# Kernel optimization log

Hardware: AMD Instinct MI355X
Metric: run time of the kernel (lower is better)

## Reference

```python
import jax, jax.numpy as jnp
import numpy as np

DIM = 1024
NUM_HEADS = 16
HEAD_DIM = DIM // NUM_HEADS
BATCH = 2
SEQ = 2048


def setup_inputs() -> dict:
    key = jax.random.key(0)
    ks = jax.random.split(key, 9)
    s = 1.0 / np.sqrt(DIM)  # torch Linear default init scale
    x = jax.random.normal(ks[0], (BATCH, SEQ, DIM), dtype=jnp.float32)
    Wq = jax.random.uniform(ks[1], (DIM, DIM), jnp.float32, -s, s)
    bq = jax.random.uniform(ks[2], (DIM,), jnp.float32, -s, s)
    Wk = jax.random.uniform(ks[3], (DIM, DIM), jnp.float32, -s, s)
    bk = jax.random.uniform(ks[4], (DIM,), jnp.float32, -s, s)
    Wv = jax.random.uniform(ks[5], (DIM, DIM), jnp.float32, -s, s)
    bv = jax.random.uniform(ks[6], (DIM,), jnp.float32, -s, s)
    Wo = jax.random.uniform(ks[7], (DIM, DIM), jnp.float32, -s, s)
    bo = jax.random.uniform(ks[8], (DIM,), jnp.float32, -s, s)
    return {"x": x, "Wq": Wq, "bq": bq, "Wk": Wk, "bk": bk,
            "Wv": Wv, "bv": bv, "Wo": Wo, "bo": bo, "enable_causal": 1}


def reference(x, Wq, bq, Wk, bk, Wv, bv, Wo, bo, enable_causal):
    B, S, D = x.shape
    H, Hd = NUM_HEADS, HEAD_DIM
    # projections (torch Linear: x @ W.T + b; W here stored as [out,in])
    q = (x @ Wq.T + bq).reshape(B, S, H, Hd).transpose(0, 2, 1, 3)  # [B,H,S,Hd]
    k = (x @ Wk.T + bk).reshape(B, S, H, Hd).transpose(0, 2, 1, 3)
    v = (x @ Wv.T + bv).reshape(B, S, H, Hd).transpose(0, 2, 1, 3)
    scores = jnp.einsum('bhqd,bhkd->bhqk', q, k) / np.sqrt(Hd)  # [B,H,S,S]
    if enable_causal:
        causal = jnp.triu(jnp.ones((S, S), dtype=bool), k=1)
        scores = jnp.where(causal, -jnp.inf, scores)
    attn = jax.nn.softmax(scores, axis=-1)
    # dropout p=0.0 -> identity (eval-mode math)
    out = jnp.einsum('bhqk,bhkd->bhqd', attn, v)  # [B,H,S,Hd]
    out = out.transpose(0, 2, 1, 3).reshape(B, S, D)
    return out @ Wo.T + bo
```

## Files before the change

### kernel.cpp

```cpp
#include <hip/hip_runtime.h>
#include <hip/hip_bf16.h>
#include <stdint.h>

typedef unsigned short u16;
typedef short bf16x8 __attribute__((ext_vector_type(8)));
typedef float f32x4 __attribute__((ext_vector_type(4)));

#define S_LEN   2048
#define D_MODEL 1024
#define NH      16
#define M_TOK   4096
#define LOG2E   1.4426950408889634f

__device__ __forceinline__ u16 f2b(float f) {
  union { float f; unsigned int u; } v; v.f = f;
  unsigned int r = v.u + 0x7FFFu + ((v.u >> 16) & 1u);
  return (u16)(r >> 16);
}

__device__ __forceinline__ float exp2_fast(float x) {
  float r;
  asm("v_exp_f32 %0, %1" : "=v"(r) : "v"(x));
  return r;
}

__device__ __forceinline__ void load_lds16(const void* g, void* l) {
  __builtin_amdgcn_global_load_lds(
      (const __attribute__((address_space(1))) void*)g,
      (__attribute__((address_space(3))) void*)l, 16, 0, 0);
}

__global__ __launch_bounds__(256) void k_convert(
    const float* __restrict__ x,
    const float* __restrict__ wq, const float* __restrict__ wk,
    const float* __restrict__ wv, const float* __restrict__ wo,
    u16* __restrict__ xb, u16* __restrict__ wb)
{
  int t = blockIdx.x * 256 + threadIdx.x;
  long e = (long)t * 8;
  const float* src; u16* dst;
  if (e < (long)M_TOK * D_MODEL) { src = x + e; dst = xb + e; }
  else {
    long we = e - (long)M_TOK * D_MODEL;
    int r = (int)(we >> 20);
    long o = we & 1048575;
    const float* ws = (r == 0) ? wq : (r == 1) ? wk : (r == 2) ? wv : wo;
    src = ws + o; dst = wb + ((long)r << 20) + o;
  }
  float4 f0 = *(const float4*)src;
  float4 f1 = *(const float4*)(src + 4);
  u16 u[8];
  u[0] = f2b(f0.x); u[1] = f2b(f0.y); u[2] = f2b(f0.z); u[3] = f2b(f0.w);
  u[4] = f2b(f1.x); u[5] = f2b(f1.y); u[6] = f2b(f1.z); u[7] = f2b(f1.w);
  *(uint4*)dst = *(const uint4*)u;
}

__device__ __forceinline__ void gemm_mainloop(
    const u16* __restrict__ At, const u16* __restrict__ Bt,
    u16* As, u16* Bs, f32x4 acc[4][4])
{
  const int tid  = threadIdx.x;
  const int lane = tid & 63;
  const int w    = tid >> 6;
  const int wr = w >> 1, wc = w & 1;
  const f32x4 fz = {0.f, 0.f, 0.f, 0.f};
  #pragma unroll
  for (int i = 0; i < 4; ++i)
    #pragma unroll
    for (int j = 0; j < 4; ++j) acc[i][j] = fz;

  const int srow = lane >> 3;
  const int sc   = lane & 7;

  for (int k0 = 0; k0 < D_MODEL; k0 += 64) {
    #pragma unroll
    for (int i = 0; i < 4; ++i) {
      int seg = i * 4 + w;
      int row = seg * 8 + srow;
      load_lds16(At + (long)row * D_MODEL + k0 + sc * 8, (char*)As + seg * 1024);
      load_lds16(Bt + (long)row * D_MODEL + k0 + sc * 8, (char*)Bs + seg * 1024);
    }
    __syncthreads();
    #pragma unroll
    for (int kc = 0; kc < 2; ++kc) {
      bf16x8 af[4], bfv[4];
      #pragma unroll
      for (int mi = 0; mi < 4; ++mi) {
        int row = wr * 64 + mi * 16 + (lane & 15);
        af[mi] = *(const bf16x8*)(As + row * 64 + kc * 32 + (lane >> 4) * 8);
      }
      #pragma unroll
      for (int ni = 0; ni < 4; ++ni) {
        int row = wc * 64 + ni * 16 + (lane & 15);
        bfv[ni] = *(const bf16x8*)(Bs + row * 64 + kc * 32 + (lane >> 4) * 8);
      }
      #pragma unroll
      for (int mi = 0; mi < 4; ++mi)
        #pragma unroll
        for (int ni = 0; ni < 4; ++ni)
          acc[mi][ni] = __builtin_amdgcn_mfma_f32_16x16x32_bf16(
              af[mi], bfv[ni], acc[mi][ni], 0, 0, 0);
    }
    __syncthreads();
  }
}

__global__ __launch_bounds__(256) void k_gemm_qkv(
    const u16* __restrict__ xb, const u16* __restrict__ wb,
    const float* __restrict__ bq, const float* __restrict__ bk,
    const float* __restrict__ bv,
    u16* __restrict__ q, u16* __restrict__ k, u16* __restrict__ v)
{
  __shared__ u16 As[128 * 64];
  __shared__ u16 Bs[128 * 64];
  const int m0   = blockIdx.x * 128;
  const int by   = blockIdx.y;
  const int proj = by >> 3;
  const int n0   = (by & 7) * 128;
  f32x4 acc[4][4];
  gemm_mainloop(xb + (long)m0 * D_MODEL,
                wb + (long)proj * 1048576 + (long)n0 * D_MODEL, As, Bs, acc);

  const int lane = threadIdx.x & 63;
  const int w    = threadIdx.x >> 6;
  const int wr = w >> 1, wc = w & 1;
  const float* bias = (proj == 0) ? bq : (proj == 1) ? bk : bv;
  u16* dst = (proj == 0) ? q : (proj == 1) ? k : v;
  const float sc = (proj == 0) ? 0.125f * LOG2E : 1.0f;
  #pragma unroll
  for (int mi = 0; mi < 4; ++mi)
    #pragma unroll
    for (int ni = 0; ni < 4; ++ni) {
      int n = n0 + wc * 64 + ni * 16 + (lane & 15);
      float bval = bias[n];
      int h = n >> 6, d = n & 63;
      #pragma unroll
      for (int r = 0; r < 4; ++r) {
        int m = m0 + wr * 64 + mi * 16 + (lane >> 4) * 4 + r;
        int b = m >> 11, s = m & 2047;
        float val = (acc[mi][ni][r] + bval) * sc;
        dst[(((long)(b * NH + h) * S_LEN + s) << 6) + d] = f2b(val);
      }
    }
}

__global__ __launch_bounds__(256) void k_transpose_v(
    const u16* __restrict__ v, u16* __restrict__ vt)
{
  __shared__ u16 t[64][65];
  const int bh = blockIdx.y;
  const int s0 = blockIdx.x * 64;
  const int tid = threadIdx.x;
  const int r = tid >> 2, cg = tid & 3;
  const u16* src = v + ((long)bh * S_LEN + s0 + r) * 64 + cg * 16;
  uint4 a = *(const uint4*)src;
  uint4 b = *(const uint4*)(src + 8);
  u16 tmp[16];
  *(uint4*)tmp = a; *(uint4*)(tmp + 8) = b;
  #pragma unroll
  for (int j = 0; j < 16; ++j) t[r][cg * 16 + j] = tmp[j];
  __syncthreads();
  u16 o[16];
  #pragma unroll
  for (int j = 0; j < 16; ++j) o[j] = t[cg * 16 + j][r];
  u16* dst = vt + ((long)bh * 64 + r) * S_LEN + s0 + cg * 16;
  *(uint4*)dst = *(const uint4*)o;
  *(uint4*)(dst + 8) = *(const uint4*)(o + 8);
}

__global__ __launch_bounds__(256) void k_attn(
    const u16* __restrict__ Q, const u16* __restrict__ K,
    const u16* __restrict__ Vt, u16* __restrict__ O,
    const int* __restrict__ causal_flag)
{
  __shared__ u16 Ks[2][64 * 64];
  __shared__ u16 Ps[4][16 * 72];

  const int tid  = threadIdx.x;
  const int lane = tid & 63;
  const int w    = tid >> 6;
  const int bid  = blockIdx.x;
  const int xcd  = bid & 7;
  const int j    = bid >> 3;
  const int kk   = j >> 5;
  const int c    = j & 31;
  const int bh   = xcd * 4 + kk;
  const int cc   = (kk & 2) ? ((c + 16) & 31) : c;
  const int qb   = (kk & 1) ? (31 - cc) : cc;
  const int q0   = qb * 64;
  const int causal = *causal_flag;

  const int l15 = lane & 15;
  const int l4  = lane >> 4;

  const u16* Kbh  = K  + (long)bh * S_LEN * 64;
  const u16* Vtbh = Vt + (long)bh * 64 * S_LEN;
  const f32x4 fz = {0.f, 0.f, 0.f, 0.f};
  const int nt = causal ? (qb + 1) : (S_LEN / 64);

  bf16x8 onesv;
  #pragma unroll
  for (int i = 0; i < 8; ++i) onesv[i] = (short)0x3F80;

  const u16 *kg0, *kg1; int lo0, lo1;
  {
    int b0 = w * 64;
    int r0 = (b0 >> 3) + (lane >> 3);
    int c0 = (lane & 7) ^ (r0 & 7);
    kg0 = Kbh + r0 * 64 + c0 * 8;  lo0 = b0 * 16;
    int b1 = 256 + w * 64;
    int r1 = (b1 >> 3) + (lane >> 3);
    int c1 = (lane & 7) ^ (r1 & 7);
    kg1 = Kbh + r1 * 64 + c1 * 8;  lo1 = b1 * 16;
  }
  #define STAGE_T(bufp, toff) do {                                   \
    load_lds16(kg0 + (toff) * 4096, (char*)(bufp) + lo0);            \
    load_lds16(kg1 + (toff) * 4096, (char*)(bufp) + lo1);            \
  } while (0)

  const u16* Vp0 = Vtbh + (long)( 0 + l15) * S_LEN + l4 * 8;
  const u16* Vp1 = Vtbh + (long)(16 + l15) * S_LEN + l4 * 8;
  const u16* Vp2 = Vtbh + (long)(32 + l15) * S_LEN + l4 * 8;
  const u16* Vp3 = Vtbh + (long)(48 + l15) * S_LEN + l4 * 8;

  const u16* Qb = Q + ((long)bh * S_LEN + q0 + w * 16) * 64;
  bf16x8 qf0 = *(const bf16x8*)(Qb + l15 * 64 +      l4 * 8);
  bf16x8 qf1 = *(const bf16x8*)(Qb + l15 * 64 + 32 + l4 * 8);

  f32x4 acc_o[4] = {fz, fz, fz, fz};
  f32x4 acc_l = fz;

  int cur = 0;
  STAGE_T(Ks[0], 0);
  asm volatile("s_waitcnt vmcnt(0)" ::: "memory");
  __builtin_amdgcn_s_barrier();

  #pragma unroll 1
  for (int t = 0; t < nt; ++t) {
    bf16x8 vf0[4], vf1[4];
    vf0[0] = *(const bf16x8*)(Vp0); vf1[0] = *(const bf16x8*)(Vp0 + 32);
    vf0[1] = *(const bf16x8*)(Vp1); vf1[1] = *(const bf16x8*)(Vp1 + 32);
    vf0[2] = *(const bf16x8*)(Vp2); vf1[2] = *(const bf16x8*)(Vp2 + 32);
    vf0[3] = *(const bf16x8*)(Vp3); vf1[3] = *(const bf16x8*)(Vp3 + 32);

    if (t + 1 < nt) STAGE_T(Ks[cur ^ 1], t + 1);

    f32x4 acc_s[4] = {fz, fz, fz, fz};
    __builtin_amdgcn_s_setprio(1);
    #pragma unroll
    for (int kc = 0; kc < 2; ++kc) {
      bf16x8 qf = kc ? qf1 : qf0;
      #pragma unroll
      for (int sub = 0; sub < 4; ++sub) {
        int krow = sub * 16 + l15;
        int cs = (kc * 4 + l4) ^ (krow & 7);
        bf16x8 kf = *(const bf16x8*)(Ks[cur] + krow * 64 + cs * 8);
        acc_s[sub] = __builtin_amdgcn_mfma_f32_16x16x32_bf16(qf, kf, acc_s[sub], 0, 0, 0);
      }
    }
    __builtin_amdgcn_s_setprio(0);

    if (causal && t == nt - 1) {
      #pragma unroll
      for (int sub = 0; sub < 4; ++sub) {
        int kvcol = t * 64 + sub * 16 + l15;
        #pragma unroll
        for (int r = 0; r < 4; ++r) {
          int qrow = q0 + w * 16 + l4 * 4 + r;
          if (kvcol > qrow) acc_s[sub][r] = -1e30f;
        }
      }
    }

    u16* P = &Ps[w][0];
    #pragma unroll
    for (int sub = 0; sub < 4; ++sub)
      #pragma unroll
      for (int r = 0; r < 4; ++r) {
        float p = exp2_fast(acc_s[sub][r]);
        P[(l4 * 4 + r) * 72 + sub * 16 + l15] = f2b(p);
      }

    asm volatile("s_waitcnt lgkmcnt(0)" ::: "memory");
    bf16x8 pf0 = *(const bf16x8*)(P + l15 * 72 +      l4 * 8);
    bf16x8 pf1 = *(const bf16x8*)(P + l15 * 72 + 32 + l4 * 8);
    __builtin_amdgcn_s_setprio(1);
    #pragma unroll
    for (int sub = 0; sub < 4; ++sub) {
      acc_o[sub] = __builtin_amdgcn_mfma_f32_16x16x32_bf16(pf0, vf0[sub], acc_o[sub], 0, 0, 0);
      acc_o[sub] = __builtin_amdgcn_mfma_f32_16x16x32_bf16(pf1, vf1[sub], acc_o[sub], 0, 0, 0);
    }
    acc_l = __builtin_amdgcn_mfma_f32_16x16x32_bf16(pf0, onesv, acc_l, 0, 0, 0);
    acc_l = __builtin_amdgcn_mfma_f32_16x16x32_bf16(pf1, onesv, acc_l, 0, 0, 0);
    __builtin_amdgcn_s_setprio(0);

    if (t + 1 < nt) {
      asm volatile("s_waitcnt vmcnt(0)" ::: "memory");
      __builtin_amdgcn_s_barrier();
      cur ^= 1;
    }
    Vp0 += 64; Vp1 += 64; Vp2 += 64; Vp3 += 64;
  }
  #undef STAGE_T

  const int b = bh >> 4, h = bh & 15;
  float rl[4];
  #pragma unroll
  for (int r = 0; r < 4; ++r) {
    asm("v_rcp_f32 %0, %1" : "=v"(rl[r]) : "v"(acc_l[r]));
  }
  #pragma unroll
  for (int sub = 0; sub < 4; ++sub)
    #pragma unroll
    for (int r = 0; r < 4; ++r) {
      int s = q0 + w * 16 + l4 * 4 + r;
      float val = acc_o[sub][r] * rl[r];
      O[((long)(b * S_LEN + s)) * D_MODEL + h * 64 + sub * 16 + l15] = f2b(val);
    }
}

__global__ __launch_bounds__(256) void k_gemm_o(
    const u16* __restrict__ ob, const u16* __restrict__ wb,
    const float* __restrict__ bo, float* __restrict__ out)
{
  __shared__ u16 As[128 * 64];
  __shared__ u16 Bs[128 * 64];
  const int m0 = blockIdx.x * 128;
  const int n0 = blockIdx.y * 128;
  f32x4 acc[4][4];
  gemm_mainloop(ob + (long)m0 * D_MODEL,
                wb + 3L * 1048576 + (long)n0 * D_MODEL, As, Bs, acc);
  const int lane = threadIdx.x & 63;
  const int w    = threadIdx.x >> 6;
  const int wr = w >> 1, wc = w & 1;
  #pragma unroll
  for (int mi = 0; mi < 4; ++mi)
    #pragma unroll
    for (int ni = 0; ni < 4; ++ni) {
      int n = n0 + wc * 64 + ni * 16 + (lane & 15);
      float bval = bo[n];
      #pragma unroll
      for (int r = 0; r < 4; ++r) {
        int m = m0 + wr * 64 + mi * 16 + (lane >> 4) * 4 + r;
        out[(long)m * D_MODEL + n] = acc[mi][ni][r] + bval;
      }
    }
}

extern "C" void kernel_launch(void* const* d_in, const int* in_sizes, int n_in,
                              void* d_out, int out_size, void* d_ws, size_t ws_size,
                              hipStream_t stream) {
  const float* x  = (const float*)d_in[0];
  const float* Wq = (const float*)d_in[1];
  const float* bq = (const float*)d_in[2];
  const float* Wk = (const float*)d_in[3];
  const float* bk = (const float*)d_in[4];
  const float* Wv = (const float*)d_in[5];
  const float* bv = (const float*)d_in[6];
  const float* Wo = (const float*)d_in[7];
  const float* bo = (const float*)d_in[8];
  const int* causal = (const int*)d_in[9];
  float* out = (float*)d_out;

  char* ws = (char*)d_ws;
  u16* xb = (u16*)(ws);
  u16* wb = (u16*)(ws + (8L  << 20));
  u16* qb = (u16*)(ws + (16L << 20));
  u16* kb = (u16*)(ws + (24L << 20));
  u16* vb = (u16*)(ws + (32L << 20));
  u16* vt = (u16*)(ws + (40L << 20));
  u16* ob = (u16*)(ws);

  k_convert   <<<4096,          256, 0, stream>>>(x, Wq, Wk, Wv, Wo, xb, wb);
  k_gemm_qkv  <<<dim3(32, 24),  256, 0, stream>>>(xb, wb, bq, bk, bv, qb, kb, vb);
  k_transpose_v<<<dim3(32, 32), 256, 0, stream>>>(vb, vt);
  k_attn      <<<1024,          256, 0, stream>>>(qb, kb, vt, ob, causal);
  k_gemm_o    <<<dim3(32, 8),   256, 0, stream>>>(ob, wb, bo, out);
}
```

Before: 251.3 us.

## Fuse V transpose into QKV epilogue and keep attention P in registers

The QKV GEMM epilogue now writes V directly in transposed layout, so the separate transpose kernel and its extra read and write pass are gone. The attention kernel drops the LDS double-buffered K staging and its barriers, loading K fragments straight from global memory into registers. It also computes S transposed (K as the A operand) and rearranges the packed bf16 probabilities across lanes with ds_bpermute instead of an LDS round trip. The cost is more global loads per wave with no sharing of K across waves, and extra cross-lane permute instructions.

```diff
diff --git a/kernel.cpp b/kernel.cpp
--- a/kernel.cpp
+++ b/kernel.cpp
@@ -5,6 +5,7 @@
 typedef unsigned short u16;
 typedef short bf16x8 __attribute__((ext_vector_type(8)));
 typedef float f32x4 __attribute__((ext_vector_type(4)));
+typedef union { unsigned w[4]; bf16x8 v; } pfrag;
 
 #define S_LEN   2048
 #define D_MODEL 1024
@@ -21,6 +22,12 @@
 __device__ __forceinline__ float exp2_fast(float x) {
   float r;
   asm("v_exp_f32 %0, %1" : "=v"(r) : "v"(x));
+  return r;
+}
+
+__device__ __forceinline__ unsigned cvt_pk(float lo, float hi) {
+  unsigned r;
+  asm("v_cvt_pk_bf16_f32 %0, %1, %2" : "=v"(r) : "v"(lo), "v"(hi));
   return r;
 }
 
@@ -109,7 +116,7 @@
     const u16* __restrict__ xb, const u16* __restrict__ wb,
     const float* __restrict__ bq, const float* __restrict__ bk,
     const float* __restrict__ bv,
-    u16* __restrict__ q, u16* __restrict__ k, u16* __restrict__ v)
+    u16* __restrict__ q, u16* __restrict__ k, u16* __restrict__ vt)
 {
   __shared__ u16 As[128 * 64];
   __shared__ u16 Bs[128 * 64];
@@ -125,47 +132,41 @@
   const int w    = threadIdx.x >> 6;
   const int wr = w >> 1, wc = w & 1;
   const float* bias = (proj == 0) ? bq : (proj == 1) ? bk : bv;
-  u16* dst = (proj == 0) ? q : (proj == 1) ? k : v;
   const float sc = (proj == 0) ? 0.125f * LOG2E : 1.0f;
-  #pragma unroll
-  for (int mi = 0; mi < 4; ++mi)
-    #pragma unroll
-    for (int ni = 0; ni < 4; ++ni) {
-      int n = n0 + wc * 64 + ni * 16 + (lane & 15);
-      float bval = bias[n];
-      int h = n >> 6, d = n & 63;
-      #pragma unroll
-      for (int r = 0; r < 4; ++r) {
-        int m = m0 + wr * 64 + mi * 16 + (lane >> 4) * 4 + r;
+
+  if (proj == 2) {
+    #pragma unroll
+    for (int mi = 0; mi < 4; ++mi)
+      #pragma unroll
+      for (int ni = 0; ni < 4; ++ni) {
+        int n = n0 + wc * 64 + ni * 16 + (lane & 15);
+        float bval = bias[n];
+        int h = n >> 6, d = n & 63;
+        int m = m0 + wr * 64 + mi * 16 + (lane >> 4) * 4;
         int b = m >> 11, s = m & 2047;
-        float val = (acc[mi][ni][r] + bval) * sc;
-        dst[(((long)(b * NH + h) * S_LEN + s) << 6) + d] = f2b(val);
-      }
-    }
-}
-
-__global__ __launch_bounds__(256) void k_transpose_v(
-    const u16* __restrict__ v, u16* __restrict__ vt)
-{
-  __shared__ u16 t[64][65];
-  const int bh = blockIdx.y;
-  const int s0 = blockIdx.x * 64;
-  const int tid = threadIdx.x;
-  const int r = tid >> 2, cg = tid & 3;
-  const u16* src = v + ((long)bh * S_LEN + s0 + r) * 64 + cg * 16;
-  uint4 a = *(const uint4*)src;
-  uint4 b = *(const uint4*)(src + 8);
-  u16 tmp[16];
-  *(uint4*)tmp = a; *(uint4*)(tmp + 8) = b;
-  #pragma unroll
-  for (int j = 0; j < 16; ++j) t[r][cg * 16 + j] = tmp[j];
-  __syncthreads();
-  u16 o[16];
-  #pragma unroll
-  for (int j = 0; j < 16; ++j) o[j] = t[cg * 16 + j][r];
-  u16* dst = vt + ((long)bh * 64 + r) * S_LEN + s0 + cg * 16;
-  *(uint4*)dst = *(const uint4*)o;
-  *(uint4*)(dst + 8) = *(const uint4*)(o + 8);
+        u16 o4[4];
+        #pragma unroll
+        for (int r = 0; r < 4; ++r) o4[r] = f2b(acc[mi][ni][r] + bval);
+        *(uint2*)&vt[((long)(b * NH + h) * 64 + d) * S_LEN + s] = *(uint2*)o4;
+      }
+  } else {
+    u16* dst = (proj == 0) ? q : k;
+    #pragma unroll
+    for (int mi = 0; mi < 4; ++mi)
+      #pragma unroll
+      for (int ni = 0; ni < 4; ++ni) {
+        int n = n0 + wc * 64 + ni * 16 + (lane & 15);
+        float bval = bias[n];
+        int h = n >> 6, d = n & 63;
+        #pragma unroll
+        for (int r = 0; r < 4; ++r) {
+          int m = m0 + wr * 64 + mi * 16 + (lane >> 4) * 4 + r;
+          int b = m >> 11, s = m & 2047;
+          float val = (acc[mi][ni][r] + bval) * sc;
+          dst[(((long)(b * NH + h) * S_LEN + s) << 6) + d] = f2b(val);
+        }
+      }
+  }
 }
 
 __global__ __launch_bounds__(256) void k_attn(
@@ -173,9 +174,6 @@
     const u16* __restrict__ Vt, u16* __restrict__ O,
     const int* __restrict__ causal_flag)
 {
-  __shared__ u16 Ks[2][64 * 64];
-  __shared__ u16 Ps[4][16 * 72];
-
   const int tid  = threadIdx.x;
   const int lane = tid & 63;
   const int w    = tid >> 6;
@@ -202,27 +200,16 @@
   #pragma unroll
   for (int i = 0; i < 8; ++i) onesv[i] = (short)0x3F80;
 
-  const u16 *kg0, *kg1; int lo0, lo1;
-  {
-    int b0 = w * 64;
-    int r0 = (b0 >> 3) + (lane >> 3);
-    int c0 = (lane & 7) ^ (r0 & 7);
-    kg0 = Kbh + r0 * 64 + c0 * 8;  lo0 = b0 * 16;
-    int b1 = 256 + w * 64;
-    int r1 = (b1 >> 3) + (lane >> 3);
-    int c1 = (lane & 7) ^ (r1 & 7);
-    kg1 = Kbh + r1 * 64 + c1 * 8;  lo1 = b1 * 16;
-  }
-  #define STAGE_T(bufp, toff) do {                                   \
-    load_lds16(kg0 + (toff) * 4096, (char*)(bufp) + lo0);            \
-    load_lds16(kg1 + (toff) * 4096, (char*)(bufp) + lo1);            \
-  } while (0)
-
+  const u16* Kp  = Kbh + l15 * 64 + l4 * 8;
   const u16* Vp0 = Vtbh + (long)( 0 + l15) * S_LEN + l4 * 8;
   const u16* Vp1 = Vtbh + (long)(16 + l15) * S_LEN + l4 * 8;
   const u16* Vp2 = Vtbh + (long)(32 + l15) * S_LEN + l4 * 8;
   const u16* Vp3 = Vtbh + (long)(48 + l15) * S_LEN + l4 * 8;
 
+  const int srcA = (((l4 & 1) * 2) * 16 + l15) * 4;
+  const int srcB = srcA + 64;
+  const bool sHi = (l4 & 2) != 0;
+
   const u16* Qb = Q + ((long)bh * S_LEN + q0 + w * 16) * 64;
   bf16x8 qf0 = *(const bf16x8*)(Qb + l15 * 64 +      l4 * 8);
   bf16x8 qf1 = *(const bf16x8*)(Qb + l15 * 64 + 32 + l4 * 8);
@@ -230,78 +217,92 @@
   f32x4 acc_o[4] = {fz, fz, fz, fz};
   f32x4 acc_l = fz;
 
-  int cur = 0;
-  STAGE_T(Ks[0], 0);
-  asm volatile("s_waitcnt vmcnt(0)" ::: "memory");
-  __builtin_amdgcn_s_barrier();
-
   #pragma unroll 1
   for (int t = 0; t < nt; ++t) {
+    bf16x8 kf0[4], kf1[4];
+    #pragma unroll
+    for (int sub = 0; sub < 4; ++sub) {
+      kf0[sub] = *(const bf16x8*)(Kp + sub * 1024);
+      kf1[sub] = *(const bf16x8*)(Kp + sub * 1024 + 32);
+    }
     bf16x8 vf0[4], vf1[4];
     vf0[0] = *(const bf16x8*)(Vp0); vf1[0] = *(const bf16x8*)(Vp0 + 32);
     vf0[1] = *(const bf16x8*)(Vp1); vf1[1] = *(const bf16x8*)(Vp1 + 32);
     vf0[2] = *(const bf16x8*)(Vp2); vf1[2] = *(const bf16x8*)(Vp2 + 32);
     vf0[3] = *(const bf16x8*)(Vp3); vf1[3] = *(const bf16x8*)(Vp3 + 32);
 
-    if (t + 1 < nt) STAGE_T(Ks[cur ^ 1], t + 1);
-
     f32x4 acc_s[4] = {fz, fz, fz, fz};
     __builtin_amdgcn_s_setprio(1);
     #pragma unroll
-    for (int kc = 0; kc < 2; ++kc) {
-      bf16x8 qf = kc ? qf1 : qf0;
-      #pragma unroll
-      for (int sub = 0; sub < 4; ++sub) {
-        int krow = sub * 16 + l15;
-        int cs = (kc * 4 + l4) ^ (krow & 7);
-        bf16x8 kf = *(const bf16x8*)(Ks[cur] + krow * 64 + cs * 8);
-        acc_s[sub] = __builtin_amdgcn_mfma_f32_16x16x32_bf16(qf, kf, acc_s[sub], 0, 0, 0);
-      }
-    }
+    for (int sub = 0; sub < 4; ++sub)
+      acc_s[sub] = __builtin_amdgcn_mfma_f32_16x16x32_bf16(kf0[sub], qf0, acc_s[sub], 0, 0, 0);
+    #pragma unroll
+    for (int sub = 0; sub < 4; ++sub)
+      acc_s[sub] = __builtin_amdgcn_mfma_f32_16x16x32_bf16(kf1[sub], qf1, acc_s[sub], 0, 0, 0);
     __builtin_amdgcn_s_setprio(0);
 
     if (causal && t == nt - 1) {
-      #pragma unroll
-      for (int sub = 0; sub < 4; ++sub) {
-        int kvcol = t * 64 + sub * 16 + l15;
+      const int qrow = q0 + w * 16 + l15;
+      #pragma unroll
+      for (int sub = 0; sub < 4; ++sub)
         #pragma unroll
         for (int r = 0; r < 4; ++r) {
-          int qrow = q0 + w * 16 + l4 * 4 + r;
-          if (kvcol > qrow) acc_s[sub][r] = -1e30f;
+          int kv = t * 64 + sub * 16 + l4 * 4 + r;
+          if (kv > qrow) acc_s[sub][r] = -1e30f;
         }
-      }
-    }
-
-    u16* P = &Ps[w][0];
-    #pragma unroll
-    for (int sub = 0; sub < 4; ++sub)
-      #pragma unroll
-      for (int r = 0; r < 4; ++r) {
-        float p = exp2_fast(acc_s[sub][r]);
-        P[(l4 * 4 + r) * 72 + sub * 16 + l15] = f2b(p);
-      }
-
-    asm volatile("s_waitcnt lgkmcnt(0)" ::: "memory");
-    bf16x8 pf0 = *(const bf16x8*)(P + l15 * 72 +      l4 * 8);
-    bf16x8 pf1 = *(const bf16x8*)(P + l15 * 72 + 32 + l4 * 8);
+    }
+
+    unsigned lo[4], hi[4];
+    #pragma unroll
+    for (int sub = 0; sub < 4; ++sub) {
+      float p0 = exp2_fast(acc_s[sub][0]);
+      float p1 = exp2_fast(acc_s[sub][1]);
+      float p2 = exp2_fast(acc_s[sub][2]);
+      float p3 = exp2_fast(acc_s[sub][3]);
+      lo[sub] = cvt_pk(p0, p1);
+      hi[sub] = cvt_pk(p2, p3);
+    }
+
+    pfrag pf0, pf1;
+    {
+      unsigned a0 = __builtin_amdgcn_ds_bpermute(srcA, (int)lo[0]);
+      unsigned a1 = __builtin_amdgcn_ds_bpermute(srcA, (int)lo[1]);
+      unsigned b0 = __builtin_amdgcn_ds_bpermute(srcA, (int)hi[0]);
+      unsigned b1 = __builtin_amdgcn_ds_bpermute(srcA, (int)hi[1]);
+      unsigned c0 = __builtin_amdgcn_ds_bpermute(srcB, (int)lo[0]);
+      unsigned c1 = __builtin_amdgcn_ds_bpermute(srcB, (int)lo[1]);
+      unsigned d0 = __builtin_amdgcn_ds_bpermute(srcB, (int)hi[0]);
+      unsigned d1 = __builtin_amdgcn_ds_bpermute(srcB, (int)hi[1]);
+      pf0.w[0] = sHi ? a1 : a0;
+      pf0.w[1] = sHi ? b1 : b0;
+      pf0.w[2] = sHi ? c1 : c0;
+      pf0.w[3] = sHi ? d1 : d0;
+      unsigned e0 = __builtin_amdgcn_ds_bpermute(srcA, (int)lo[2]);
+      unsigned e1 = __builtin_amdgcn_ds_bpermute(srcA, (int)lo[3]);
+      unsigned f0 = __builtin_amdgcn_ds_bpermute(srcA, (int)hi[2]);
+      unsigned f1 = __builtin_amdgcn_ds_bpermute(srcA, (int)hi[3]);
+      unsigned g0 = __builtin_amdgcn_ds_bpermute(srcB, (int)lo[2]);
+      unsigned g1 = __builtin_amdgcn_ds_bpermute(srcB, (int)lo[3]);
+      unsigned h0 = __builtin_amdgcn_ds_bpermute(srcB, (int)hi[2]);
+      unsigned h1 = __builtin_amdgcn_ds_bpermute(srcB, (int)hi[3]);
+      pf1.w[0] = sHi ? e1 : e0;
+      pf1.w[1] = sHi ? f1 : f0;
+      pf1.w[2] = sHi ? g1 : g0;
+      pf1.w[3] = sHi ? h1 : h0;
+    }
+
     __builtin_amdgcn_s_setprio(1);
     #pragma unroll
     for (int sub = 0; sub < 4; ++sub) {
-      acc_o[sub] = __builtin_amdgcn_mfma_f32_16x16x32_bf16(pf0, vf0[sub], acc_o[sub], 0, 0, 0);
-      acc_o[sub] = __builtin_amdgcn_mfma_f32_16x16x32_bf16(pf1, vf1[sub], acc_o[sub], 0, 0, 0);
-    }
-    acc_l = __builtin_amdgcn_mfma_f32_16x16x32_bf16(pf0, onesv, acc_l, 0, 0, 0);
-    acc_l = __builtin_amdgcn_mfma_f32_16x16x32_bf16(pf1, onesv, acc_l, 0, 0, 0);
+      acc_o[sub] = __builtin_amdgcn_mfma_f32_16x16x32_bf16(pf0.v, vf0[sub], acc_o[sub], 0, 0, 0);
+      acc_o[sub] = __builtin_amdgcn_mfma_f32_16x16x32_bf16(pf1.v, vf1[sub], acc_o[sub], 0, 0, 0);
+    }
+    acc_l = __builtin_amdgcn_mfma_f32_16x16x32_bf16(pf0.v, onesv, acc_l, 0, 0, 0);
+    acc_l = __builtin_amdgcn_mfma_f32_16x16x32_bf16(pf1.v, onesv, acc_l, 0, 0, 0);
     __builtin_amdgcn_s_setprio(0);
 
-    if (t + 1 < nt) {
-      asm volatile("s_waitcnt vmcnt(0)" ::: "memory");
-      __builtin_amdgcn_s_barrier();
-      cur ^= 1;
-    }
-    Vp0 += 64; Vp1 += 64; Vp2 += 64; Vp3 += 64;
-  }
-  #undef STAGE_T
+    Kp += 4096; Vp0 += 64; Vp1 += 64; Vp2 += 64; Vp3 += 64;
+  }
 
   const int b = bh >> 4, h = bh & 15;
   float rl[4];
@@ -367,13 +368,11 @@
   u16* wb = (u16*)(ws + (8L  << 20));
   u16* qb = (u16*)(ws + (16L << 20));
   u16* kb = (u16*)(ws + (24L << 20));
-  u16* vb = (u16*)(ws + (32L << 20));
-  u16* vt = (u16*)(ws + (40L << 20));
+  u16* vt = (u16*)(ws + (32L << 20));
   u16* ob = (u16*)(ws);
 
   k_convert   <<<4096,          256, 0, stream>>>(x, Wq, Wk, Wv, Wo, xb, wb);
-  k_gemm_qkv  <<<dim3(32, 24),  256, 0, stream>>>(xb, wb, bq, bk, bv, qb, kb, vb);
-  k_transpose_v<<<dim3(32, 32), 256, 0, stream>>>(vb, vt);
+  k_gemm_qkv  <<<dim3(32, 24),  256, 0, stream>>>(xb, wb, bq, bk, bv, qb, kb, vt);
   k_attn      <<<1024,          256, 0, stream>>>(qb, kb, vt, ob, causal);
   k_gemm_o    <<<dim3(32, 8),   256, 0, stream>>>(ob, wb, bo, out);
 }
```

Result: slower. 285.4 us (+13.6%).
